# Performance work log

Hardware: AMD Instinct MI355X
Metric: run time of the kernel (lower is better)

Reference implementation:

```python
import jax, jax.numpy as jnp
import numpy as np

N_DIM = 512
HEADS = 8
NUM_EXPERTS = 65536
NUM_KEYS = 256      # sqrt(NUM_EXPERTS)
DIM_KEY = 256       # N_DIM // 2
TOPK = 16           # num_experts_per_head (also product_key_topk)
SCALE = 0.02


def setup_inputs() -> dict:
    key = jax.random.key(0)
    k0, k1, k2, k3, k4 = jax.random.split(key, 5)
    x = jax.random.normal(k0, (1, 2048, N_DIM), dtype=jnp.float32)
    W_q = jax.random.normal(k1, (N_DIM, 2 * HEADS * DIM_KEY), dtype=jnp.float32) * SCALE
    keys = jax.random.normal(k2, (HEADS, NUM_KEYS, 2, DIM_KEY), dtype=jnp.float32) * SCALE
    down_embed = jax.random.normal(k3, (NUM_EXPERTS, N_DIM), dtype=jnp.float32) * SCALE
    up_embed = jax.random.normal(k4, (NUM_EXPERTS, N_DIM), dtype=jnp.float32) * SCALE
    return {"x": x, "W_q": W_q, "keys": keys, "down_embed": down_embed, "up_embed": up_embed}


def reference(x, W_q, keys, down_embed, up_embed):
    b, n, d = x.shape
    # queries: [b,n,2*h*dk] -> [2,b,n,h,dk]
    q = (x @ W_q).reshape(b, n, 2, HEADS, DIM_KEY).transpose(2, 0, 1, 3, 4)
    # similarity against product keys: [2,b,n,h,num_keys]
    sim = jnp.einsum('pbnhd,hkpd->pbnhk', q, keys)
    sx, ix = jax.lax.top_k(sim[0], TOPK)   # [b,n,h,TOPK]
    sy, iy = jax.lax.top_k(sim[1], TOPK)
    # cartesian product of the two top-k sets -> [b,n,h,TOPK*TOPK]
    all_scores = (sx[..., :, None] + sy[..., None, :]).reshape(b, n, HEADS, TOPK * TOPK)
    scores, pk_idx = jax.lax.top_k(all_scores, TOPK)  # [b,n,h,TOPK]
    # NOTE: original module indexes embeddings with pk_idx (flat top-k positions),
    # reproduced faithfully here.
    w_down = down_embed[pk_idx]  # [b,n,h,TOPK,d]
    w_up = up_embed[pk_idx]      # [b,n,h,TOPK,d]
    h = jnp.einsum('bnd,bnhkd->bnhk', x, w_down)
    h = jax.nn.gelu(h, approximate=False)
    h = jax.nn.softmax(scores, axis=-1) * h
    return jnp.einsum('bnhk,bnhkd->bnd', h, w_up)
```

## Files before the change

kernel.cpp:

```cpp
#include <hip/hip_runtime.h>
#include <math.h>

#define N_TOK 2048
#define NDIM 512
#define HEADS 8
#define TOPK 16
#define QCOLS 4096
#define MCOLS 4352

typedef __attribute__((ext_vector_type(8))) _Float16 f16x8;
typedef __attribute__((ext_vector_type(4))) float f32x4;

__device__ __forceinline__ unsigned short f32_to_f16(float f) {
    _Float16 h = (_Float16)f;
    return __builtin_bit_cast(unsigned short, h);
}
__device__ __forceinline__ float f16_to_f32(unsigned short u) {
    return (float)__builtin_bit_cast(_Float16, u);
}
__device__ __forceinline__ void gl_lds16(const void* g, void* l) {
    __builtin_amdgcn_global_load_lds(
        (const __attribute__((address_space(1))) void*)g,
        (__attribute__((address_space(3))) void*)l, 16, 0, 0);
}

__global__ __launch_bounds__(256) void kPrep(const float* __restrict__ x,
                                             const float* __restrict__ down,
                                             unsigned short* __restrict__ xh,
                                             unsigned short* __restrict__ xl,
                                             unsigned short* __restrict__ Mth,
                                             unsigned short* __restrict__ Mtl) {
    const int bid = blockIdx.x;
    const int tid = threadIdx.x;
    if (bid < 1024) {
        const int i = bid * 256 + tid;
        float4 v = reinterpret_cast<const float4*>(x)[i];
        float vv[4] = {v.x, v.y, v.z, v.w};
        ushort4 h, lo;
        unsigned short* hp = &h.x; unsigned short* lp = &lo.x;
        #pragma unroll
        for (int t = 0; t < 4; ++t) {
            unsigned short hh = f32_to_f16(vv[t]);
            hp[t] = hh;
            lp[t] = f32_to_f16(vv[t] - f16_to_f32(hh));
        }
        reinterpret_cast<ushort4*>(xh)[i] = h;
        reinterpret_cast<ushort4*>(xl)[i] = lo;
    } else {
        const int e = bid - 1024;
        const int d0 = tid * 2;
        float2 v = *reinterpret_cast<const float2*>(&down[(size_t)e * NDIM + d0]);
        ushort2 h, lo;
        unsigned short h0 = f32_to_f16(v.x);
        unsigned short h1 = f32_to_f16(v.y);
        h.x = h0; h.y = h1;
        lo.x = f32_to_f16(v.x - f16_to_f32(h0));
        lo.y = f32_to_f16(v.y - f16_to_f32(h1));
        *reinterpret_cast<ushort2*>(&Mth[(size_t)(QCOLS + e) * NDIM + d0]) = h;
        *reinterpret_cast<ushort2*>(&Mtl[(size_t)(QCOLS + e) * NDIM + d0]) = lo;
    }
}

__global__ __launch_bounds__(256) void k1_combine(const float* __restrict__ Wq,
                                                  const float* __restrict__ keys,
                                                  unsigned short* __restrict__ Mth,
                                                  unsigned short* __restrict__ Mtl) {
    __shared__ float As[16][64];
    __shared__ float Bs[16][64];
    const int ph = blockIdx.z;
    const int p = ph >> 3, h = ph & 7;
    const int off = p * 2048 + h * 256;
    const int c0 = blockIdx.x * 64;
    const int k0 = blockIdx.y * 64;
    const int tid = threadIdx.x;
    const int lr = tid >> 2;
    const int ld4 = (tid & 3) * 4;
    const int tr = tid >> 4, tc = tid & 15;
    float acc[4][4] = {};
    for (int d0 = 0; d0 < 256; d0 += 16) {
        float4 av = *reinterpret_cast<const float4*>(&Wq[(size_t)(c0 + lr) * QCOLS + off + d0 + ld4]);
        float4 bv = *reinterpret_cast<const float4*>(&keys[(size_t)((h * 256 + (k0 + lr)) * 2 + p) * 256 + d0 + ld4]);
        __syncthreads();
        As[ld4 + 0][lr] = av.x; As[ld4 + 1][lr] = av.y; As[ld4 + 2][lr] = av.z; As[ld4 + 3][lr] = av.w;
        Bs[ld4 + 0][lr] = bv.x; Bs[ld4 + 1][lr] = bv.y; Bs[ld4 + 2][lr] = bv.z; Bs[ld4 + 3][lr] = bv.w;
        __syncthreads();
        #pragma unroll
        for (int kk = 0; kk < 16; ++kk) {
            float4 a = *reinterpret_cast<const float4*>(&As[kk][tr * 4]);
            float4 b = *reinterpret_cast<const float4*>(&Bs[kk][tc * 4]);
            float aa[4] = {a.x, a.y, a.z, a.w}, bb[4] = {b.x, b.y, b.z, b.w};
            #pragma unroll
            for (int i = 0; i < 4; ++i)
                #pragma unroll
                for (int j = 0; j < 4; ++j) acc[i][j] += aa[i] * bb[j];
        }
    }
    #pragma unroll
    for (int j = 0; j < 4; ++j) {
        const int col = off + k0 + tc * 4 + j;
        ushort4 h4, l4;
        unsigned short* hp = &h4.x; unsigned short* lp = &l4.x;
        #pragma unroll
        for (int i = 0; i < 4; ++i) {
            float v = acc[i][j];
            unsigned short hh = f32_to_f16(v);
            hp[i] = hh;
            lp[i] = f32_to_f16(v - f16_to_f32(hh));
        }
        *reinterpret_cast<ushort4*>(&Mth[(size_t)col * NDIM + c0 + tr * 4]) = h4;
        *reinterpret_cast<ushort4*>(&Mtl[(size_t)col * NDIM + c0 + tr * 4]) = l4;
    }
}

#define BM 64
#define BN 128
#define BK 64
__global__ __launch_bounds__(256, 4) void k2_mfma(const unsigned short* __restrict__ xh,
                                                  const unsigned short* __restrict__ xl,
                                                  const unsigned short* __restrict__ Mth,
                                                  const unsigned short* __restrict__ Mtl,
                                                  float* __restrict__ C) {
    __shared__ __align__(16) unsigned short ldsAh[BM * BK];
    __shared__ __align__(16) unsigned short ldsAl[BM * BK];
    __shared__ __align__(16) unsigned short ldsBh[BN * BK];
    __shared__ __align__(16) unsigned short ldsBl[BN * BK];
    const int tid = threadIdx.x;
    const int w = tid >> 6, l = tid & 63;
    const int row0 = blockIdx.x * BM;
    const int col0 = blockIdx.y * BN;
    const int wm = w >> 1, wn = w & 1;
    f32x4 acc[2][4] = {};

    for (int s = 0; s < 8; ++s) {
        const int kk = s * BK;
        __syncthreads();
        #pragma unroll
        for (int t = 0; t < 2; ++t) {
            const int qq = w * 2048 + t * 1024 + l * 16;
            const int row = qq >> 7;
            const int bs = (qq & 127) ^ ((row & 7) << 4);
            const size_t gsrc = (size_t)(row0 + row) * NDIM + kk + (bs >> 1);
            gl_lds16(xh + gsrc, (char*)ldsAh + w * 2048 + t * 1024);
            gl_lds16(xl + gsrc, (char*)ldsAl + w * 2048 + t * 1024);
        }
        #pragma unroll
        for (int t = 0; t < 4; ++t) {
            const int qq = w * 4096 + t * 1024 + l * 16;
            const int row = qq >> 7;
            const int bs = (qq & 127) ^ ((row & 7) << 4);
            const size_t gsrc = (size_t)(col0 + row) * NDIM + kk + (bs >> 1);
            gl_lds16(Mth + gsrc, (char*)ldsBh + w * 4096 + t * 1024);
            gl_lds16(Mtl + gsrc, (char*)ldsBl + w * 4096 + t * 1024);
        }
        __syncthreads();
        #pragma unroll
        for (int kc = 0; kc < 2; ++kc) {
            f16x8 ah[2], al[2], bh[4], bl[4];
            #pragma unroll
            for (int mi = 0; mi < 2; ++mi) {
                const int row = wm * 32 + mi * 16 + (l & 15);
                const int b = (kc * 64 + (l >> 4) * 16) ^ ((row & 7) << 4);
                ah[mi] = *(const f16x8*)((const char*)ldsAh + row * 128 + b);
                al[mi] = *(const f16x8*)((const char*)ldsAl + row * 128 + b);
            }
            #pragma unroll
            for (int nj = 0; nj < 4; ++nj) {
                const int row = wn * 64 + nj * 16 + (l & 15);
                const int b = (kc * 64 + (l >> 4) * 16) ^ ((row & 7) << 4);
                bh[nj] = *(const f16x8*)((const char*)ldsBh + row * 128 + b);
                bl[nj] = *(const f16x8*)((const char*)ldsBl + row * 128 + b);
            }
            #pragma unroll
            for (int mi = 0; mi < 2; ++mi)
                #pragma unroll
                for (int nj = 0; nj < 4; ++nj) {
                    acc[mi][nj] = __builtin_amdgcn_mfma_f32_16x16x32_f16(ah[mi], bh[nj], acc[mi][nj], 0, 0, 0);
                    acc[mi][nj] = __builtin_amdgcn_mfma_f32_16x16x32_f16(ah[mi], bl[nj], acc[mi][nj], 0, 0, 0);
                    acc[mi][nj] = __builtin_amdgcn_mfma_f32_16x16x32_f16(al[mi], bh[nj], acc[mi][nj], 0, 0, 0);
                }
        }
    }
    #pragma unroll
    for (int mi = 0; mi < 2; ++mi)
        #pragma unroll
        for (int nj = 0; nj < 4; ++nj)
            #pragma unroll
            for (int r = 0; r < 4; ++r) {
                const int row = row0 + wm * 32 + mi * 16 + (l >> 4) * 4 + r;
                const int col = col0 + wn * 64 + nj * 16 + (l & 15);
                C[(size_t)row * MCOLS + col] = acc[mi][nj][r];
            }
}

__device__ const unsigned short CAND_TBL[32] = {
    0x0100, 0x0302, 0x0504, 0x0706, 0x0908, 0x0B0A, 0x0D0C, 0x0F0E,
    0x1110, 0x1312, 0x1514, 0x1716,
    0x2120, 0x2322, 0x3024, 0x3231, 0x4033, 0x4241,
    0x5150, 0x6160, 0x7170,
    0x9080, 0xB0A0, 0xD0C0, 0xF0E0,
    0xFFFF, 0xFFFF, 0xFFFF, 0xFFFF, 0xFFFF, 0xFFFF, 0xFFFF
};

__device__ __forceinline__ float sel16(const float a[16], int i) {
    float b0 = (i & 1) ? a[1] : a[0];
    float b1 = (i & 1) ? a[3] : a[2];
    float b2 = (i & 1) ? a[5] : a[4];
    float b3 = (i & 1) ? a[7] : a[6];
    float b4 = (i & 1) ? a[9] : a[8];
    float b5 = (i & 1) ? a[11] : a[10];
    float b6 = (i & 1) ? a[13] : a[12];
    float b7 = (i & 1) ? a[15] : a[14];
    float c0 = (i & 2) ? b1 : b0;
    float c1 = (i & 2) ? b3 : b2;
    float c2 = (i & 2) ? b5 : b4;
    float c3 = (i & 2) ? b7 : b6;
    float d0 = (i & 4) ? c1 : c0;
    float d1 = (i & 4) ? c3 : c2;
    return (i & 8) ? d1 : d0;
}

__global__ __launch_bounds__(256) void k3_sel(const float* __restrict__ sim,
                                              float* __restrict__ W) {
    __shared__ unsigned long long ckey[8][50];
    __shared__ float winval[8][16];
    __shared__ int winflat[8][16];
    __shared__ int Wrow[256];

    const int tid = threadIdx.x;
    const int n = blockIdx.x;
    const int h = tid >> 5;
    const int lam = tid & 15;
    const int p = (tid >> 4) & 1;

    Wrow[tid] = 0;

    const float* s = sim + (size_t)n * MCOLS + p * 2048 + h * 256 + lam * 16;
    float v[16];
    #pragma unroll
    for (int c = 0; c < 4; ++c) {
        float4 t = *reinterpret_cast<const float4*>(s + c * 4);
        v[c * 4 + 0] = t.x; v[c * 4 + 1] = t.y; v[c * 4 + 2] = t.z; v[c * 4 + 3] = t.w;
    }

    #pragma unroll
    for (int k = 2; k <= 16; k <<= 1)
        #pragma unroll
        for (int j = k >> 1; j > 0; j >>= 1)
            #pragma unroll
            for (int i = 0; i < 16; ++i) {
                const int l2 = i ^ j;
                if (l2 > i) {
                    const bool asc = ((i & k) == 0);
                    const float lo = fminf(v[i], v[l2]), hi = fmaxf(v[i], v[l2]);
                    v[i] = asc ? lo : hi;
                    v[l2] = asc ? hi : lo;
                }
            }

    #pragma unroll
    for (int lvl = 1; lvl <= 8; lvl <<= 1) {
        float m[16];
        #pragma unroll
        for (int q = 0; q < 16; ++q)
            m[q] = fmaxf(v[q], __shfl_xor(v[15 - q], lvl));
        #pragma unroll
        for (int j = 8; j > 0; j >>= 1)
            #pragma unroll
            for (int i = 0; i < 16; ++i) {
                const int l2 = i ^ j;
                if (l2 > i) {
                    const float lo = fminf(m[i], m[l2]), hi = fmaxf(m[i], m[l2]);
                    m[i] = lo; m[l2] = hi;
                }
            }
        #pragma unroll
        for (int q = 0; q < 16; ++q) v[q] = m[q];
    }

    float other[16];
    #pragma unroll
    for (int q = 0; q < 16; ++q) other[q] = __shfl_xor(v[q], 16);
    const bool isP1 = (tid & 16) != 0;
    float sxd[16], syd[16];
    #pragma unroll
    for (int q = 0; q < 16; ++q) {
        const float own = v[15 - q], oth = other[15 - q];
        sxd[q] = isP1 ? oth : own;
        syd[q] = isP1 ? own : oth;
    }

    const int lc = tid & 31;
    const unsigned int cw = CAND_TBL[lc];
    unsigned long long mykey[2]; float myval[2]; int myflat[2]; int myrank[2] = {0, 0};
    #pragma unroll
    for (int u = 0; u < 2; ++u) {
        const int fl = (cw >> (8 * u)) & 0xFF;
        const float sv = sel16(sxd, fl >> 4) + sel16(syd, fl & 15);
        const unsigned int uv = __float_as_uint(sv);
        const unsigned int mo = (uv & 0x80000000u) ? ~uv : (uv | 0x80000000u);
        mykey[u] = ((unsigned long long)mo << 8) | (unsigned long long)(255 - fl);
        myval[u] = sv; myflat[u] = fl;
        const int slot = lc * 2 + u;
        if (slot < 50) ckey[h][slot] = mykey[u];
    }
    __syncthreads();
    for (int kk = 0; kk < 50; ++kk) {
        const unsigned long long ok = ckey[h][kk];
        myrank[0] += (ok > mykey[0]) ? 1 : 0;
        myrank[1] += (ok > mykey[1]) ? 1 : 0;
    }
    #pragma unroll
    for (int u = 0; u < 2; ++u)
        if (myrank[u] < 16) { winval[h][myrank[u]] = myval[u]; winflat[h][myrank[u]] = myflat[u]; }
    __syncthreads();

    if (!(tid & 16)) {
        const float sc = winval[h][lam];
        const float m0 = winval[h][0];
        float e = expf(sc - m0);
        float esum = e;
        #pragma unroll
        for (int off = 1; off < 16; off <<= 1) esum += __shfl_xor(esum, off);
        const int fl = winflat[h][lam];
        const float hv = sim[(size_t)n * MCOLS + QCOLS + fl];
        const float g = 0.5f * hv * (1.0f + erff(hv * 0.70710678118654752f));
        const float w = (e / esum) * g;
        atomicAdd(&Wrow[fl], __float2int_rn(w * 4194304.0f));
    }
    __syncthreads();
    W[(size_t)n * 256 + tid] = (float)Wrow[tid] * (1.0f / 4194304.0f);
}

__global__ __launch_bounds__(256) void k5_out(const float* __restrict__ W,
                                              const float* __restrict__ up,
                                              float* __restrict__ out) {
    __shared__ float As[16][64];
    __shared__ float Bs[16][64];
    const int row0 = blockIdx.x * 64;
    const int col0 = blockIdx.y * 64;
    const int tid = threadIdx.x;
    const int ar = tid >> 2, ak = (tid & 3) * 4;
    const int bk = tid >> 4, bc = (tid & 15) * 4;
    const int tr = tid >> 4, tc = tid & 15;
    float acc[4][4] = {};
    for (int k0 = 0; k0 < 256; k0 += 16) {
        float4 av = *reinterpret_cast<const float4*>(&W[(size_t)(row0 + ar) * 256 + k0 + ak]);
        float4 bv = *reinterpret_cast<const float4*>(&up[(size_t)(k0 + bk) * NDIM + col0 + bc]);
        __syncthreads();
        As[ak + 0][ar] = av.x; As[ak + 1][ar] = av.y; As[ak + 2][ar] = av.z; As[ak + 3][ar] = av.w;
        *reinterpret_cast<float4*>(&Bs[bk][bc]) = bv;
        __syncthreads();
        #pragma unroll
        for (int kk = 0; kk < 16; ++kk) {
            float4 a = *(const float4*)&As[kk][tr * 4];
            float4 b = *(const float4*)&Bs[kk][tc * 4];
            float aa[4] = {a.x, a.y, a.z, a.w}, bb[4] = {b.x, b.y, b.z, b.w};
            #pragma unroll
            for (int i = 0; i < 4; ++i)
                #pragma unroll
                for (int j = 0; j < 4; ++j) acc[i][j] += aa[i] * bb[j];
        }
    }
    #pragma unroll
    for (int i = 0; i < 4; ++i) {
        float4 o = {acc[i][0], acc[i][1], acc[i][2], acc[i][3]};
        *reinterpret_cast<float4*>(&out[(size_t)(row0 + tr * 4 + i) * NDIM + col0 + tc * 4]) = o;
    }
}

extern "C" void kernel_launch(void* const* d_in, const int* in_sizes, int n_in,
                              void* d_out, int out_size, void* d_ws, size_t ws_size,
                              hipStream_t stream) {
    const float* x    = (const float*)d_in[0];
    const float* Wq   = (const float*)d_in[1];
    const float* keys = (const float*)d_in[2];
    const float* down = (const float*)d_in[3];
    const float* up   = (const float*)d_in[4];
    float* out = (float*)d_out;

    char* ws = (char*)d_ws;
    unsigned short* Mth = (unsigned short*)(ws);
    unsigned short* Mtl = (unsigned short*)(ws + 4456448);
    unsigned short* xh  = (unsigned short*)(ws + 8912896);
    unsigned short* xl  = (unsigned short*)(ws + 11010048);
    float* sim          = (float*)(ws + 13107200);
    float* W            = (float*)(ws + 48758784);

    kPrep<<<1280, 256, 0, stream>>>(x, down, xh, xl, Mth, Mtl);
    k1_combine<<<dim3(8, 4, 16), 256, 0, stream>>>(Wq, keys, Mth, Mtl);
    k2_mfma<<<dim3(32, 34), 256, 0, stream>>>(xh, xl, Mth, Mtl, sim);
    k3_sel<<<2048, 256, 0, stream>>>(sim, W);
    k5_out<<<dim3(32, 8), 256, 0, stream>>>(W, up, out);
}
```

Measured before the change: 112.7 us.

## Double-buffer k2 MFMA LDS tiles and prefetch global loads in k1/k5

```diff
diff --git a/kernel.cpp b/kernel.cpp
--- a/kernel.cpp
+++ b/kernel.cpp
@@ -77,13 +77,19 @@
     const int ld4 = (tid & 3) * 4;
     const int tr = tid >> 4, tc = tid & 15;
     float acc[4][4] = {};
+    const float* ap = &Wq[(size_t)(c0 + lr) * QCOLS + off + ld4];
+    const float* bp = &keys[(size_t)((h * 256 + (k0 + lr)) * 2 + p) * 256 + ld4];
+    float4 av = *reinterpret_cast<const float4*>(ap);
+    float4 bv = *reinterpret_cast<const float4*>(bp);
     for (int d0 = 0; d0 < 256; d0 += 16) {
-        float4 av = *reinterpret_cast<const float4*>(&Wq[(size_t)(c0 + lr) * QCOLS + off + d0 + ld4]);
-        float4 bv = *reinterpret_cast<const float4*>(&keys[(size_t)((h * 256 + (k0 + lr)) * 2 + p) * 256 + d0 + ld4]);
         __syncthreads();
         As[ld4 + 0][lr] = av.x; As[ld4 + 1][lr] = av.y; As[ld4 + 2][lr] = av.z; As[ld4 + 3][lr] = av.w;
         Bs[ld4 + 0][lr] = bv.x; Bs[ld4 + 1][lr] = bv.y; Bs[ld4 + 2][lr] = bv.z; Bs[ld4 + 3][lr] = bv.w;
         __syncthreads();
+        if (d0 + 16 < 256) {
+            av = *reinterpret_cast<const float4*>(ap + d0 + 16);
+            bv = *reinterpret_cast<const float4*>(bp + d0 + 16);
+        }
         #pragma unroll
         for (int kk = 0; kk < 16; ++kk) {
             float4 a = *reinterpret_cast<const float4*>(&As[kk][tr * 4]);
@@ -114,16 +120,16 @@
 
 #define BM 64
 #define BN 128
-#define BK 64
-__global__ __launch_bounds__(256, 4) void k2_mfma(const unsigned short* __restrict__ xh,
+#define BK 32
+#define ABYTES 8192
+#define BBYTES 16384
+#define BUFBYTES 24576
+__global__ __launch_bounds__(256, 3) void k2_mfma(const unsigned short* __restrict__ xh,
                                                   const unsigned short* __restrict__ xl,
                                                   const unsigned short* __restrict__ Mth,
                                                   const unsigned short* __restrict__ Mtl,
                                                   float* __restrict__ C) {
-    __shared__ __align__(16) unsigned short ldsAh[BM * BK];
-    __shared__ __align__(16) unsigned short ldsAl[BM * BK];
-    __shared__ __align__(16) unsigned short ldsBh[BN * BK];
-    __shared__ __align__(16) unsigned short ldsBl[BN * BK];
+    __shared__ __align__(16) char lds[2 * BUFBYTES];
     const int tid = threadIdx.x;
     const int w = tid >> 6, l = tid & 63;
     const int row0 = blockIdx.x * BM;
@@ -131,54 +137,61 @@
     const int wm = w >> 1, wn = w & 1;
     f32x4 acc[2][4] = {};
 
-    for (int s = 0; s < 8; ++s) {
+    auto stage = [&](int buf, int s) {
         const int kk = s * BK;
+        char* base = lds + buf * BUFBYTES;
+        #pragma unroll
+        for (int t = 0; t < 2; ++t) {
+            const int q = w * 2048 + t * 1024 + l * 16;
+            const int r = q >> 7;
+            const int bsw = (q & 127) ^ ((r & 7) << 4);
+            const unsigned short* src = (bsw < 64)
+                ? xh + (size_t)(row0 + r) * NDIM + kk + (bsw >> 1)
+                : xl + (size_t)(row0 + r) * NDIM + kk + ((bsw - 64) >> 1);
+            gl_lds16(src, base + w * 2048 + t * 1024);
+        }
+        #pragma unroll
+        for (int t = 0; t < 4; ++t) {
+            const int q = w * 4096 + t * 1024 + l * 16;
+            const int r = q >> 7;
+            const int bsw = (q & 127) ^ ((r & 7) << 4);
+            const unsigned short* src = (bsw < 64)
+                ? Mth + (size_t)(col0 + r) * NDIM + kk + (bsw >> 1)
+                : Mtl + (size_t)(col0 + r) * NDIM + kk + ((bsw - 64) >> 1);
+            gl_lds16(src, base + ABYTES + w * 4096 + t * 1024);
+        }
+    };
+
+    stage(0, 0);
+    __syncthreads();
+    for (int s = 0; s < 16; ++s) {
+        if (s + 1 < 16) stage((s + 1) & 1, s + 1);
+        const char* base = lds + (s & 1) * BUFBYTES;
+        const int bq = (l >> 4) * 16;
+        f16x8 ah[2], al[2], bh[4], bl[4];
+        #pragma unroll
+        for (int mi = 0; mi < 2; ++mi) {
+            const int ra = wm * 32 + mi * 16 + (l & 15);
+            const int swz = (ra & 7) << 4;
+            ah[mi] = *(const f16x8*)(base + ra * 128 + (bq ^ swz));
+            al[mi] = *(const f16x8*)(base + ra * 128 + ((bq + 64) ^ swz));
+        }
+        #pragma unroll
+        for (int nj = 0; nj < 4; ++nj) {
+            const int rb = wn * 64 + nj * 16 + (l & 15);
+            const int swz = (rb & 7) << 4;
+            bh[nj] = *(const f16x8*)(base + ABYTES + rb * 128 + (bq ^ swz));
+            bl[nj] = *(const f16x8*)(base + ABYTES + rb * 128 + ((bq + 64) ^ swz));
+        }
+        #pragma unroll
+        for (int mi = 0; mi < 2; ++mi)
+            #pragma unroll
+            for (int nj = 0; nj < 4; ++nj) {
+                acc[mi][nj] = __builtin_amdgcn_mfma_f32_16x16x32_f16(ah[mi], bh[nj], acc[mi][nj], 0, 0, 0);
+                acc[mi][nj] = __builtin_amdgcn_mfma_f32_16x16x32_f16(ah[mi], bl[nj], acc[mi][nj], 0, 0, 0);
+                acc[mi][nj] = __builtin_amdgcn_mfma_f32_16x16x32_f16(al[mi], bh[nj], acc[mi][nj], 0, 0, 0);
+            }
         __syncthreads();
-        #pragma unroll
-        for (int t = 0; t < 2; ++t) {
-            const int qq = w * 2048 + t * 1024 + l * 16;
-            const int row = qq >> 7;
-            const int bs = (qq & 127) ^ ((row & 7) << 4);
-            const size_t gsrc = (size_t)(row0 + row) * NDIM + kk + (bs >> 1);
-            gl_lds16(xh + gsrc, (char*)ldsAh + w * 2048 + t * 1024);
-            gl_lds16(xl + gsrc, (char*)ldsAl + w * 2048 + t * 1024);
-        }
-        #pragma unroll
-        for (int t = 0; t < 4; ++t) {
-            const int qq = w * 4096 + t * 1024 + l * 16;
-            const int row = qq >> 7;
-            const int bs = (qq & 127) ^ ((row & 7) << 4);
-            const size_t gsrc = (size_t)(col0 + row) * NDIM + kk + (bs >> 1);
-            gl_lds16(Mth + gsrc, (char*)ldsBh + w * 4096 + t * 1024);
-            gl_lds16(Mtl + gsrc, (char*)ldsBl + w * 4096 + t * 1024);
-        }
-        __syncthreads();
-        #pragma unroll
-        for (int kc = 0; kc < 2; ++kc) {
-            f16x8 ah[2], al[2], bh[4], bl[4];
-            #pragma unroll
-            for (int mi = 0; mi < 2; ++mi) {
-                const int row = wm * 32 + mi * 16 + (l & 15);
-                const int b = (kc * 64 + (l >> 4) * 16) ^ ((row & 7) << 4);
-                ah[mi] = *(const f16x8*)((const char*)ldsAh + row * 128 + b);
-                al[mi] = *(const f16x8*)((const char*)ldsAl + row * 128 + b);
-            }
-            #pragma unroll
-            for (int nj = 0; nj < 4; ++nj) {
-                const int row = wn * 64 + nj * 16 + (l & 15);
-                const int b = (kc * 64 + (l >> 4) * 16) ^ ((row & 7) << 4);
-                bh[nj] = *(const f16x8*)((const char*)ldsBh + row * 128 + b);
-                bl[nj] = *(const f16x8*)((const char*)ldsBl + row * 128 + b);
-            }
-            #pragma unroll
-            for (int mi = 0; mi < 2; ++mi)
-                #pragma unroll
-                for (int nj = 0; nj < 4; ++nj) {
-                    acc[mi][nj] = __builtin_amdgcn_mfma_f32_16x16x32_f16(ah[mi], bh[nj], acc[mi][nj], 0, 0, 0);
-                    acc[mi][nj] = __builtin_amdgcn_mfma_f32_16x16x32_f16(ah[mi], bl[nj], acc[mi][nj], 0, 0, 0);
-                    acc[mi][nj] = __builtin_amdgcn_mfma_f32_16x16x32_f16(al[mi], bh[nj], acc[mi][nj], 0, 0, 0);
-                }
-        }
     }
     #pragma unroll
     for (int mi = 0; mi < 2; ++mi)
@@ -334,37 +347,45 @@
 __global__ __launch_bounds__(256) void k5_out(const float* __restrict__ W,
                                               const float* __restrict__ up,
                                               float* __restrict__ out) {
-    __shared__ float As[16][64];
+    __shared__ float As[16][32];
     __shared__ float Bs[16][64];
-    const int row0 = blockIdx.x * 64;
+    const int row0 = blockIdx.x * 32;
     const int col0 = blockIdx.y * 64;
     const int tid = threadIdx.x;
-    const int ar = tid >> 2, ak = (tid & 3) * 4;
+    const int ar = tid & 31, ak = (tid >> 5) * 2;
     const int bk = tid >> 4, bc = (tid & 15) * 4;
-    const int tr = tid >> 4, tc = tid & 15;
-    float acc[4][4] = {};
+    const int r0 = (tid >> 4) * 2, c0 = (tid & 15) * 4;
+    float acc[2][4] = {};
+    const float* wp = &W[(size_t)(row0 + ar) * 256 + ak];
+    const float* up0 = &up[(size_t)bk * NDIM + col0 + bc];
+    float2 a2 = *reinterpret_cast<const float2*>(wp);
+    float4 b4 = *reinterpret_cast<const float4*>(up0);
     for (int k0 = 0; k0 < 256; k0 += 16) {
-        float4 av = *reinterpret_cast<const float4*>(&W[(size_t)(row0 + ar) * 256 + k0 + ak]);
-        float4 bv = *reinterpret_cast<const float4*>(&up[(size_t)(k0 + bk) * NDIM + col0 + bc]);
         __syncthreads();
-        As[ak + 0][ar] = av.x; As[ak + 1][ar] = av.y; As[ak + 2][ar] = av.z; As[ak + 3][ar] = av.w;
-        *reinterpret_cast<float4*>(&Bs[bk][bc]) = bv;
+        As[ak + 0][ar] = a2.x;
+        As[ak + 1][ar] = a2.y;
+        *reinterpret_cast<float4*>(&Bs[bk][bc]) = b4;
         __syncthreads();
+        if (k0 + 16 < 256) {
+            a2 = *reinterpret_cast<const float2*>(wp + k0 + 16);
+            b4 = *reinterpret_cast<const float4*>(up0 + (size_t)16 * NDIM + (size_t)k0 * NDIM);
+        }
         #pragma unroll
         for (int kk = 0; kk < 16; ++kk) {
-            float4 a = *(const float4*)&As[kk][tr * 4];
-            float4 b = *(const float4*)&Bs[kk][tc * 4];
-            float aa[4] = {a.x, a.y, a.z, a.w}, bb[4] = {b.x, b.y, b.z, b.w};
-            #pragma unroll
-            for (int i = 0; i < 4; ++i)
-                #pragma unroll
-                for (int j = 0; j < 4; ++j) acc[i][j] += aa[i] * bb[j];
-        }
-    }
-    #pragma unroll
-    for (int i = 0; i < 4; ++i) {
+            const float a0 = As[kk][r0], a1 = As[kk][r0 + 1];
+            float4 b = *reinterpret_cast<const float4*>(&Bs[kk][c0]);
+            float bb[4] = {b.x, b.y, b.z, b.w};
+            #pragma unroll
+            for (int j = 0; j < 4; ++j) {
+                acc[0][j] += a0 * bb[j];
+                acc[1][j] += a1 * bb[j];
+            }
+        }
+    }
+    #pragma unroll
+    for (int i = 0; i < 2; ++i) {
         float4 o = {acc[i][0], acc[i][1], acc[i][2], acc[i][3]};
-        *reinterpret_cast<float4*>(&out[(size_t)(row0 + tr * 4 + i) * NDIM + col0 + tc * 4]) = o;
+        *reinterpret_cast<float4*>(&out[(size_t)(row0 + r0 + i) * NDIM + col0 + c0]) = o;
     }
 }
 
@@ -390,5 +411,5 @@
     k1_combine<<<dim3(8, 4, 16), 256, 0, stream>>>(Wq, keys, Mth, Mtl);
     k2_mfma<<<dim3(32, 34), 256, 0, stream>>>(xh, xl, Mth, Mtl, sim);
     k3_sel<<<2048, 256, 0, stream>>>(sim, W);
-    k5_out<<<dim3(32, 8), 256, 0, stream>>>(W, up, out);
-}
+    k5_out<<<dim3(64, 8), 256, 0, stream>>>(W, up, out);
+}
```

Result: faster. 105.2 us (-6.6%).
